# Kernel tuning notes

Measured on AMD Instinct MI355X. Metric: run time of the kernel, lower is better.

## Reference

```python
import jax, jax.numpy as jnp
import numpy as np

N_NODES = 50000
N_EDGES = 800000
IN_DIM = 128
HID = 64
NUM_GRAPHS = 64


def _gcn_conv(x, W, b, src, dst, num_nodes):
    """PyG GCNConv: out = D^-1/2 (A+I) D^-1/2 (x W) + b, messages scattered to dst."""
    h = x @ W  # [N, out]
    ones = jnp.ones((src.shape[0],), dtype=x.dtype)
    # degree at target nodes, self-loop adds 1
    deg = jax.ops.segment_sum(ones, dst, num_segments=num_nodes) + 1.0
    dinv = jax.lax.rsqrt(deg)  # [N]
    norm = dinv[src] * dinv[dst]  # [E]
    msgs = h[src] * norm[:, None]  # [E, out] gather-scale
    agg = jax.ops.segment_sum(msgs, dst, num_segments=num_nodes)  # scatter-add
    # self-loop contribution: norm_ii = dinv[i]^2
    agg = agg + h * (dinv * dinv)[:, None]
    return agg + b


def setup_inputs() -> dict:
    key = jax.random.key(0)
    k = jax.random.split(key, 10)
    x = jax.random.normal(k[0], (N_NODES, IN_DIM), dtype=jnp.float32)
    edge_index = jax.random.randint(k[1], (2, N_EDGES), 0, N_NODES, dtype=jnp.int32)
    batch = jnp.sort(jax.random.randint(k[2], (N_NODES,), 0, NUM_GRAPHS, dtype=jnp.int32))
    # Glorot-ish params
    W1 = jax.random.normal(k[3], (IN_DIM, HID), dtype=jnp.float32) / np.sqrt(IN_DIM)
    b1 = jnp.zeros((HID,), dtype=jnp.float32)
    W2 = jax.random.normal(k[4], (HID, HID), dtype=jnp.float32) / np.sqrt(HID)
    b2 = jnp.zeros((HID,), dtype=jnp.float32)
    Wlin = jax.random.normal(k[5], (HID, 1), dtype=jnp.float32) / np.sqrt(HID)
    blin = jnp.zeros((1,), dtype=jnp.float32)
    return {"x": x, "edge_index": edge_index, "batch": batch,
            "W1": W1, "b1": b1, "W2": W2, "b2": b2, "Wlin": Wlin, "blin": blin}


def reference(x, edge_index, batch, W1, b1, W2, b2, Wlin, blin):
    src, dst = edge_index[0], edge_index[1]
    h = _gcn_conv(x, W1, b1, src, dst, N_NODES)
    h = jax.nn.relu(h)  # dropout is identity in eval mode
    h = _gcn_conv(h, W2, b2, src, dst, N_NODES)
    h = jax.nn.relu(h)
    # global mean pool per graph
    sums = jax.ops.segment_sum(h, batch, num_segments=NUM_GRAPHS)  # [G, HID]
    cnts = jax.ops.segment_sum(jnp.ones((N_NODES,), h.dtype), batch, num_segments=NUM_GRAPHS)
    pooled = sums / jnp.maximum(cnts, 1.0)[:, None]
    return pooled @ Wlin + blin  # [G, 1]
```

## Files before the change

kernel.cpp:

```cpp
#include <hip/hip_runtime.h>
#include <hip/hip_fp16.h>

#define N_NODES 50000
#define N_EDGES 800000
#define IN_DIM 128
#define HID 64
#define NUM_GRAPHS 64
#define POOL_BLOCKS 512
#define NB 196
#define NBLK 256

__device__ inline float4 load_h4(const __half* p) {
    const __half2* q = (const __half2*)p;
    float2 a = __half22float2(q[0]);
    float2 b = __half22float2(q[1]);
    return make_float4(a.x, a.y, b.x, b.y);
}
__device__ inline void store_h4(__half* p, float4 v) {
    __half2* q = (__half2*)p;
    q[0] = __floats2half2_rn(v.x, v.y);
    q[1] = __floats2half2_rn(v.z, v.w);
}

__global__ __launch_bounds__(256) void hist_kernel(const int* __restrict__ dst, int* __restrict__ hist_g) {
    __shared__ int h[NB];
    int tid = threadIdx.x;
    for (int i = tid; i < NB; i += 256) h[i] = 0;
    __syncthreads();
    const int NI = N_EDGES / 4;
    for (int i = blockIdx.x * 256 + tid; i < NI; i += NBLK * 256) {
        int4 d = ((const int4*)dst)[i];
        atomicAdd(&h[d.x >> 8], 1);
        atomicAdd(&h[d.y >> 8], 1);
        atomicAdd(&h[d.z >> 8], 1);
        atomicAdd(&h[d.w >> 8], 1);
    }
    __syncthreads();
    for (int i = tid; i < NB; i += 256) hist_g[i * NBLK + blockIdx.x] = h[i];
}

__global__ __launch_bounds__(1024) void scan2_kernel(const int* __restrict__ in, int* __restrict__ pos,
                                                     int* __restrict__ offs) {
    __shared__ int wsum[16];
    __shared__ int tot_s;
    int tid = threadIdx.x;
    int lane = tid & 63, wid = tid >> 6;
    int carry = 0;
    const int L = NB * NBLK;
    for (int base = 0; base < L; base += 4096) {
        int idx = base + tid * 4;
        int v0 = 0, v1 = 0, v2 = 0, v3 = 0;
        if (idx < L) { int4 v = *(const int4*)&in[idx]; v0 = v.x; v1 = v.y; v2 = v.z; v3 = v.w; }
        int s0 = v0, s1 = s0 + v1, s2 = s1 + v2, s3 = s2 + v3;
        int inc = s3;
        #pragma unroll
        for (int d = 1; d < 64; d <<= 1) { int t = __shfl_up(inc, d, 64); if (lane >= d) inc += t; }
        if (lane == 63) wsum[wid] = inc;
        __syncthreads();
        if (tid < 16) {
            int wv = wsum[tid], winc = wv;
            #pragma unroll
            for (int d = 1; d < 16; d <<= 1) { int t = __shfl_up(winc, d, 16); if (tid >= d) winc += t; }
            wsum[tid] = winc - wv;
            if (tid == 15) tot_s = winc;
        }
        __syncthreads();
        int excl = carry + wsum[wid] + inc - s3;
        if (idx < L) { int4 o; o.x = excl; o.y = excl + s0; o.z = excl + s1; o.w = excl + s2; *(int4*)&pos[idx] = o; }
        carry += tot_s;
    }
    if (tid == 0) offs[N_NODES] = N_EDGES;
}

__global__ __launch_bounds__(256) void bin_kernel(const int* __restrict__ src, const int* __restrict__ dst,
                                                  const int* __restrict__ pos, int* __restrict__ binned) {
    __shared__ int cur[NB];
    int tid = threadIdx.x;
    for (int i = tid; i < NB; i += 256) cur[i] = pos[i * NBLK + blockIdx.x];
    __syncthreads();
    const int NI = N_EDGES / 4;
    for (int i = blockIdx.x * 256 + tid; i < NI; i += NBLK * 256) {
        int4 s = ((const int4*)src)[i];
        int4 d = ((const int4*)dst)[i];
        int p0 = atomicAdd(&cur[d.x >> 8], 1); binned[p0] = (s.x & 0xFFFF) | ((d.x & 255) << 16);
        int p1 = atomicAdd(&cur[d.y >> 8], 1); binned[p1] = (s.y & 0xFFFF) | ((d.y & 255) << 16);
        int p2 = atomicAdd(&cur[d.z >> 8], 1); binned[p2] = (s.z & 0xFFFF) | ((d.z & 255) << 16);
        int p3 = atomicAdd(&cur[d.w >> 8], 1); binned[p3] = (s.w & 0xFFFF) | ((d.w & 255) << 16);
    }
}

__global__ __launch_bounds__(256) void build_kernel(const int* __restrict__ binned, const int* __restrict__ pos,
                                                    int* __restrict__ offs, float* __restrict__ dinv,
                                                    int* __restrict__ csr_src) {
    __shared__ int cnt[256];
    __shared__ int excl[256];
    __shared__ int rnk[256];
    __shared__ int wtot[4];
    int b = blockIdx.x, tid = threadIdx.x;
    int base = pos[b * NBLK];
    int end  = (b == NB - 1) ? N_EDGES : pos[(b + 1) * NBLK];
    cnt[tid] = 0; rnk[tid] = 0;
    __syncthreads();
    for (int j = base + tid; j < end; j += 256) atomicAdd(&cnt[(binned[j] >> 16) & 255], 1);
    __syncthreads();
    int v = cnt[tid];
    int lane = tid & 63, wid = tid >> 6;
    int inc = v;
    #pragma unroll
    for (int d = 1; d < 64; d <<= 1) { int t = __shfl_up(inc, d, 64); if (lane >= d) inc += t; }
    if (lane == 63) wtot[wid] = inc;
    __syncthreads();
    if (tid == 0) {
        int a = 0;
        for (int w = 0; w < 4; w++) { int t = wtot[w]; wtot[w] = a; a += t; }
    }
    __syncthreads();
    excl[tid] = wtot[wid] + inc - v;
    int node = b * 256 + tid;
    if (node < N_NODES) {
        offs[node] = base + excl[tid];
        dinv[node] = rsqrtf((float)v + 1.0f);
    }
    __syncthreads();
    for (int j = base + tid; j < end; j += 256) {
        int e = binned[j];
        int l = (e >> 16) & 255;
        int r = atomicAdd(&rnk[l], 1);
        csr_src[base + excl[l] + r] = e & 0xFFFF;
    }
}

template <int K, typename TIN>
__global__ __launch_bounds__(256) void gemm_kernel(const TIN* __restrict__ A, const float* __restrict__ W,
                                                   const float* __restrict__ dinv,
                                                   __half* __restrict__ out, int nRows) {
    constexpr int KP = K + 4;
    __shared__ float xs[32 * KP];
    __shared__ float ws[K * 68];
    int tid = threadIdx.x;
    int node0 = blockIdx.x * 32;
    for (int i = tid; i < K * 16; i += 256) {
        int k = i >> 4, c4 = (i & 15) * 4;
        *(float4*)&ws[k * 68 + c4] = *(const float4*)&W[k * 64 + c4];
    }
    constexpr int K4 = K / 4;
    for (int i = tid; i < 32 * K4; i += 256) {
        int n = i / K4, k4 = i % K4;
        int gn = node0 + n;
        float4 v;
        if (gn < nRows) {
            if constexpr (sizeof(TIN) == 4) v = *(const float4*)&A[(size_t)gn * K + k4 * 4];
            else                            v = load_h4((const __half*)&A[(size_t)gn * K + k4 * 4]);
        } else v = make_float4(0.f, 0.f, 0.f, 0.f);
        *(float4*)&xs[n * KP + k4 * 4] = v;
    }
    __syncthreads();
    int tx4 = (tid & 15) * 4, ty = tid >> 4;
    int n0 = ty * 2;
    float acc[2][4] = {};
    for (int k = 0; k < K; k += 4) {
        float4 xv0 = *(const float4*)&xs[(n0 + 0) * KP + k];
        float4 xv1 = *(const float4*)&xs[(n0 + 1) * KP + k];
        #define GSTEP(X0, X1, KK) { \
            float4 wr = *(const float4*)&ws[(KK) * 68 + tx4]; \
            acc[0][0] += (X0) * wr.x; acc[0][1] += (X0) * wr.y; acc[0][2] += (X0) * wr.z; acc[0][3] += (X0) * wr.w; \
            acc[1][0] += (X1) * wr.x; acc[1][1] += (X1) * wr.y; acc[1][2] += (X1) * wr.z; acc[1][3] += (X1) * wr.w; }
        GSTEP(xv0.x, xv1.x, k + 0)
        GSTEP(xv0.y, xv1.y, k + 1)
        GSTEP(xv0.z, xv1.z, k + 2)
        GSTEP(xv0.w, xv1.w, k + 3)
        #undef GSTEP
    }
    #pragma unroll
    for (int i = 0; i < 2; i++) {
        int gn = node0 + n0 + i;
        if (gn < nRows) {
            float sc = dinv[gn];
            store_h4(&out[(size_t)gn * 64 + tx4],
                     make_float4(acc[i][0] * sc, acc[i][1] * sc, acc[i][2] * sc, acc[i][3] * sc));
        }
    }
}

__global__ __launch_bounds__(256) void agg_kernel(const __half* __restrict__ hd, const int* __restrict__ offs,
                                                  const int* __restrict__ csr_src,
                                                  const float* __restrict__ dinv, const float* __restrict__ bias,
                                                  __half* __restrict__ out) {
    int lane = threadIdx.x & 63;
    int node = blockIdx.x * 4 + (threadIdx.x >> 6);
    if (node >= N_NODES) return;
    int q = lane >> 4;
    int cc = (lane & 15) * 4;
    float4 acc = make_float4(0.f, 0.f, 0.f, 0.f);
    int beg = offs[node], end = offs[node + 1];
    #pragma unroll 2
    for (int j = beg + q; j < end; j += 4) {
        int s = csr_src[j];
        float4 hv = load_h4(&hd[(size_t)s * 64 + cc]);
        acc.x += hv.x; acc.y += hv.y; acc.z += hv.z; acc.w += hv.w;
    }
    #pragma unroll
    for (int m = 16; m <= 32; m <<= 1) {
        acc.x += __shfl_xor(acc.x, m, 64);
        acc.y += __shfl_xor(acc.y, m, 64);
        acc.z += __shfl_xor(acc.z, m, 64);
        acc.w += __shfl_xor(acc.w, m, 64);
    }
    if (q == 0) {
        float di = dinv[node];
        float4 hn = load_h4(&hd[(size_t)node * 64 + cc]);
        const float4 bv = *(const float4*)&bias[cc];
        float4 r;
        r.x = fmaxf(fmaf(di, acc.x + hn.x, bv.x), 0.0f);
        r.y = fmaxf(fmaf(di, acc.y + hn.y, bv.y), 0.0f);
        r.z = fmaxf(fmaf(di, acc.z + hn.z, bv.z), 0.0f);
        r.w = fmaxf(fmaf(di, acc.w + hn.w, bv.w), 0.0f);
        store_h4(&out[(size_t)node * 64 + cc], r);
    }
}

__global__ __launch_bounds__(256) void pool_kernel(const __half* __restrict__ y, const int* __restrict__ batch,
                                                   const float* __restrict__ Wlin,
                                                   float* __restrict__ gpart) {
    __shared__ float lsum[NUM_GRAPHS];
    __shared__ float lcnt[NUM_GRAPHS];
    int tid = threadIdx.x;
    if (tid < NUM_GRAPHS) { lsum[tid] = 0.0f; lcnt[tid] = 0.0f; }
    __syncthreads();
    int lane = tid & 63, wid = tid >> 6;
    int q = lane >> 4;
    int l16 = lane & 15;
    int cc = l16 * 4;
    float4 wl = *(const float4*)&Wlin[cc];
    int stride = gridDim.x * 16;
    #pragma unroll 2
    for (int node = blockIdx.x * 16 + wid * 4 + q; node < N_NODES; node += stride) {
        float4 v = load_h4(&y[(size_t)node * 64 + cc]);
        float d = v.x * wl.x + v.y * wl.y + v.z * wl.z + v.w * wl.w;
        #pragma unroll
        for (int m = 1; m < 16; m <<= 1) d += __shfl_xor(d, m, 64);
        if (l16 == 0) {
            int g = batch[node];
            atomicAdd(&lsum[g], d);
            atomicAdd(&lcnt[g], 1.0f);
        }
    }
    __syncthreads();
    if (tid < NUM_GRAPHS) {
        gpart[(size_t)blockIdx.x * (2 * NUM_GRAPHS) + tid] = lsum[tid];
        gpart[(size_t)blockIdx.x * (2 * NUM_GRAPHS) + NUM_GRAPHS + tid] = lcnt[tid];
    }
}

__global__ __launch_bounds__(1024) void final_kernel(const float* __restrict__ gpart, const float* __restrict__ blin,
                                                     float* __restrict__ out) {
    __shared__ float rs[1024];
    __shared__ float rc[1024];
    int tid = threadIdx.x;
    int g = tid & 63;
    int c = tid >> 6;
    float s = 0.0f, cn = 0.0f;
    for (int b = c; b < POOL_BLOCKS; b += 16) {
        s  += gpart[(size_t)b * (2 * NUM_GRAPHS) + g];
        cn += gpart[(size_t)b * (2 * NUM_GRAPHS) + NUM_GRAPHS + g];
    }
    rs[tid] = s; rc[tid] = cn;
    __syncthreads();
    if (c == 0) {
        float ts = 0.0f, tc = 0.0f;
        #pragma unroll
        for (int k = 0; k < 16; k++) { ts += rs[k * 64 + g]; tc += rc[k * 64 + g]; }
        out[g] = ts / fmaxf(tc, 1.0f) + blin[0];
    }
}

extern "C" void kernel_launch(void* const* d_in, const int* in_sizes, int n_in,
                              void* d_out, int out_size, void* d_ws, size_t ws_size,
                              hipStream_t stream) {
    const float* x    = (const float*)d_in[0];
    const int*   ei   = (const int*)d_in[1];
    const int*   batch= (const int*)d_in[2];
    const float* W1   = (const float*)d_in[3];
    const float* b1   = (const float*)d_in[4];
    const float* W2   = (const float*)d_in[5];
    const float* b2   = (const float*)d_in[6];
    const float* Wlin = (const float*)d_in[7];
    const float* blin = (const float*)d_in[8];
    float* out = (float*)d_out;
    const int* srcA = ei;
    const int* dstA = ei + N_EDGES;

    char* p = (char*)d_ws;
    auto alloc = [&](size_t n) { char* r = p; p += (n + 255) & ~(size_t)255; return r; };
    int*    hist_g  = (int*)alloc((size_t)NB * NBLK * 4);
    int*    pos     = (int*)alloc((size_t)NB * NBLK * 4);
    int*    offs    = (int*)alloc((size_t)(N_NODES + 1) * 4);
    int*    binned  = (int*)alloc((size_t)N_EDGES * 4);
    int*    csr_src = (int*)alloc((size_t)N_EDGES * 4);
    float*  dinv    = (float*)alloc((size_t)N_NODES * 4);
    float*  gpart   = (float*)alloc((size_t)POOL_BLOCKS * 2 * NUM_GRAPHS * 4);
    __half* bufA    = (__half*)alloc((size_t)N_NODES * 64 * 2);
    __half* bufB    = (__half*)alloc((size_t)N_NODES * 64 * 2);

    hist_kernel<<<NBLK, 256, 0, stream>>>(dstA, hist_g);
    scan2_kernel<<<1, 1024, 0, stream>>>(hist_g, pos, offs);
    bin_kernel<<<NBLK, 256, 0, stream>>>(srcA, dstA, pos, binned);
    build_kernel<<<NB, 256, 0, stream>>>(binned, pos, offs, dinv, csr_src);

    gemm_kernel<IN_DIM, float><<<(N_NODES + 31) / 32, 256, 0, stream>>>(x, W1, dinv, bufA, N_NODES);
    agg_kernel<<<(N_NODES + 3) / 4, 256, 0, stream>>>(bufA, offs, csr_src, dinv, b1, bufB);
    gemm_kernel<HID, __half><<<(N_NODES + 31) / 32, 256, 0, stream>>>(bufB, W2, dinv, bufA, N_NODES);
    agg_kernel<<<(N_NODES + 3) / 4, 256, 0, stream>>>(bufA, offs, csr_src, dinv, b2, bufB);

    pool_kernel<<<POOL_BLOCKS, 256, 0, stream>>>(bufB, batch, Wlin, gpart);
    final_kernel<<<1, 1024, 0, stream>>>(gpart, blin, out);
}
```

Before: 229.9 us.

## Fuse second aggregation with mean pooling and enlarge GEMM register tiles

```diff
diff --git a/kernel.cpp b/kernel.cpp
--- a/kernel.cpp
+++ b/kernel.cpp
@@ -6,7 +6,7 @@
 #define IN_DIM 128
 #define HID 64
 #define NUM_GRAPHS 64
-#define POOL_BLOCKS 512
+#define AGGP_BLOCKS 2048
 #define NB 196
 #define NBLK 256
 
@@ -134,50 +134,57 @@
 __global__ __launch_bounds__(256) void gemm_kernel(const TIN* __restrict__ A, const float* __restrict__ W,
                                                    const float* __restrict__ dinv,
                                                    __half* __restrict__ out, int nRows) {
-    constexpr int KP = K + 4;
-    __shared__ float xs[32 * KP];
-    __shared__ float ws[K * 68];
-    int tid = threadIdx.x;
-    int node0 = blockIdx.x * 32;
-    for (int i = tid; i < K * 16; i += 256) {
-        int k = i >> 4, c4 = (i & 15) * 4;
-        *(float4*)&ws[k * 68 + c4] = *(const float4*)&W[k * 64 + c4];
-    }
-    constexpr int K4 = K / 4;
-    for (int i = tid; i < 32 * K4; i += 256) {
-        int n = i / K4, k4 = i % K4;
-        int gn = node0 + n;
-        float4 v;
-        if (gn < nRows) {
-            if constexpr (sizeof(TIN) == 4) v = *(const float4*)&A[(size_t)gn * K + k4 * 4];
-            else                            v = load_h4((const __half*)&A[(size_t)gn * K + k4 * 4]);
-        } else v = make_float4(0.f, 0.f, 0.f, 0.f);
-        *(float4*)&xs[n * KP + k4 * 4] = v;
-    }
-    __syncthreads();
-    int tx4 = (tid & 15) * 4, ty = tid >> 4;
-    int n0 = ty * 2;
-    float acc[2][4] = {};
-    for (int k = 0; k < K; k += 4) {
-        float4 xv0 = *(const float4*)&xs[(n0 + 0) * KP + k];
-        float4 xv1 = *(const float4*)&xs[(n0 + 1) * KP + k];
-        #define GSTEP(X0, X1, KK) { \
-            float4 wr = *(const float4*)&ws[(KK) * 68 + tx4]; \
-            acc[0][0] += (X0) * wr.x; acc[0][1] += (X0) * wr.y; acc[0][2] += (X0) * wr.z; acc[0][3] += (X0) * wr.w; \
-            acc[1][0] += (X1) * wr.x; acc[1][1] += (X1) * wr.y; acc[1][2] += (X1) * wr.z; acc[1][3] += (X1) * wr.w; }
-        GSTEP(xv0.x, xv1.x, k + 0)
-        GSTEP(xv0.y, xv1.y, k + 1)
-        GSTEP(xv0.z, xv1.z, k + 2)
-        GSTEP(xv0.w, xv1.w, k + 3)
-        #undef GSTEP
+    constexpr int KB = 64;
+    __shared__ float xs[KB * 132];
+    __shared__ float ws[KB * 68];
+    int tid = threadIdx.x;
+    int node0 = blockIdx.x * 128;
+    int tx = tid & 7, ty = tid >> 3;
+    int c0 = tx * 8, n0 = ty * 4;
+    float acc[4][8] = {};
+    for (int kb = 0; kb < K; kb += KB) {
+        for (int i = tid; i < KB * 16; i += 256) {
+            int k = i >> 4, c4 = (i & 15) * 4;
+            *(float4*)&ws[k * 68 + c4] = *(const float4*)&W[(size_t)(kb + k) * 64 + c4];
+        }
+        for (int i = tid; i < 128 * (KB / 4); i += 256) {
+            int n = i / (KB / 4), k4 = (i % (KB / 4)) * 4;
+            int gn = node0 + n;
+            float4 v;
+            if (gn < nRows) {
+                if constexpr (sizeof(TIN) == 4) v = *(const float4*)&A[(size_t)gn * K + kb + k4];
+                else                            v = load_h4((const __half*)&A[(size_t)gn * K + kb + k4]);
+            } else v = make_float4(0.f, 0.f, 0.f, 0.f);
+            xs[(k4 + 0) * 132 + n] = v.x;
+            xs[(k4 + 1) * 132 + n] = v.y;
+            xs[(k4 + 2) * 132 + n] = v.z;
+            xs[(k4 + 3) * 132 + n] = v.w;
+        }
+        __syncthreads();
+        for (int k = 0; k < KB; k++) {
+            float4 xv = *(const float4*)&xs[k * 132 + n0];
+            float4 w0 = *(const float4*)&ws[k * 68 + c0];
+            float4 w1 = *(const float4*)&ws[k * 68 + c0 + 4];
+            #define NODE_FMA(i, X) \
+                acc[i][0] += (X) * w0.x; acc[i][1] += (X) * w0.y; acc[i][2] += (X) * w0.z; acc[i][3] += (X) * w0.w; \
+                acc[i][4] += (X) * w1.x; acc[i][5] += (X) * w1.y; acc[i][6] += (X) * w1.z; acc[i][7] += (X) * w1.w;
+            NODE_FMA(0, xv.x)
+            NODE_FMA(1, xv.y)
+            NODE_FMA(2, xv.z)
+            NODE_FMA(3, xv.w)
+            #undef NODE_FMA
+        }
+        __syncthreads();
     }
     #pragma unroll
-    for (int i = 0; i < 2; i++) {
+    for (int i = 0; i < 4; i++) {
         int gn = node0 + n0 + i;
         if (gn < nRows) {
             float sc = dinv[gn];
-            store_h4(&out[(size_t)gn * 64 + tx4],
+            store_h4(&out[(size_t)gn * 64 + c0],
                      make_float4(acc[i][0] * sc, acc[i][1] * sc, acc[i][2] * sc, acc[i][3] * sc));
+            store_h4(&out[(size_t)gn * 64 + c0 + 4],
+                     make_float4(acc[i][4] * sc, acc[i][5] * sc, acc[i][6] * sc, acc[i][7] * sc));
         }
     }
 }
@@ -219,9 +226,11 @@
     }
 }
 
-__global__ __launch_bounds__(256) void pool_kernel(const __half* __restrict__ y, const int* __restrict__ batch,
-                                                   const float* __restrict__ Wlin,
-                                                   float* __restrict__ gpart) {
+__global__ __launch_bounds__(256) void aggpool_kernel(const __half* __restrict__ hd, const int* __restrict__ offs,
+                                                      const int* __restrict__ csr_src,
+                                                      const float* __restrict__ dinv, const float* __restrict__ bias,
+                                                      const int* __restrict__ batch, const float* __restrict__ Wlin,
+                                                      float* __restrict__ gpart) {
     __shared__ float lsum[NUM_GRAPHS];
     __shared__ float lcnt[NUM_GRAPHS];
     int tid = threadIdx.x;
@@ -229,20 +238,41 @@
     __syncthreads();
     int lane = tid & 63, wid = tid >> 6;
     int q = lane >> 4;
-    int l16 = lane & 15;
-    int cc = l16 * 4;
-    float4 wl = *(const float4*)&Wlin[cc];
-    int stride = gridDim.x * 16;
-    #pragma unroll 2
-    for (int node = blockIdx.x * 16 + wid * 4 + q; node < N_NODES; node += stride) {
-        float4 v = load_h4(&y[(size_t)node * 64 + cc]);
-        float d = v.x * wl.x + v.y * wl.y + v.z * wl.z + v.w * wl.w;
+    int cc = (lane & 15) * 4;
+    const float4 wl = *(const float4*)&Wlin[cc];
+    int stride = gridDim.x * 4;
+    for (int node = blockIdx.x * 4 + wid; node < N_NODES; node += stride) {
+        float4 acc = make_float4(0.f, 0.f, 0.f, 0.f);
+        int beg = offs[node], end = offs[node + 1];
+        #pragma unroll 2
+        for (int j = beg + q; j < end; j += 4) {
+            int s = csr_src[j];
+            float4 hv = load_h4(&hd[(size_t)s * 64 + cc]);
+            acc.x += hv.x; acc.y += hv.y; acc.z += hv.z; acc.w += hv.w;
+        }
         #pragma unroll
-        for (int m = 1; m < 16; m <<= 1) d += __shfl_xor(d, m, 64);
-        if (l16 == 0) {
-            int g = batch[node];
-            atomicAdd(&lsum[g], d);
-            atomicAdd(&lcnt[g], 1.0f);
+        for (int m = 16; m <= 32; m <<= 1) {
+            acc.x += __shfl_xor(acc.x, m, 64);
+            acc.y += __shfl_xor(acc.y, m, 64);
+            acc.z += __shfl_xor(acc.z, m, 64);
+            acc.w += __shfl_xor(acc.w, m, 64);
+        }
+        if (q == 0) {
+            float di = dinv[node];
+            float4 hn = load_h4(&hd[(size_t)node * 64 + cc]);
+            const float4 bv = *(const float4*)&bias[cc];
+            float rx = fmaxf(fmaf(di, acc.x + hn.x, bv.x), 0.0f);
+            float ry = fmaxf(fmaf(di, acc.y + hn.y, bv.y), 0.0f);
+            float rz = fmaxf(fmaf(di, acc.z + hn.z, bv.z), 0.0f);
+            float rw = fmaxf(fmaf(di, acc.w + hn.w, bv.w), 0.0f);
+            float d = rx * wl.x + ry * wl.y + rz * wl.z + rw * wl.w;
+            #pragma unroll
+            for (int m = 1; m < 16; m <<= 1) d += __shfl_xor(d, m, 64);
+            if ((lane & 15) == 0) {
+                int g = batch[node];
+                atomicAdd(&lsum[g], d);
+                atomicAdd(&lcnt[g], 1.0f);
+            }
         }
     }
     __syncthreads();
@@ -260,7 +290,7 @@
     int g = tid & 63;
     int c = tid >> 6;
     float s = 0.0f, cn = 0.0f;
-    for (int b = c; b < POOL_BLOCKS; b += 16) {
+    for (int b = c; b < AGGP_BLOCKS; b += 16) {
         s  += gpart[(size_t)b * (2 * NUM_GRAPHS) + g];
         cn += gpart[(size_t)b * (2 * NUM_GRAPHS) + NUM_GRAPHS + g];
     }
@@ -298,7 +328,7 @@
     int*    binned  = (int*)alloc((size_t)N_EDGES * 4);
     int*    csr_src = (int*)alloc((size_t)N_EDGES * 4);
     float*  dinv    = (float*)alloc((size_t)N_NODES * 4);
-    float*  gpart   = (float*)alloc((size_t)POOL_BLOCKS * 2 * NUM_GRAPHS * 4);
+    float*  gpart   = (float*)alloc((size_t)AGGP_BLOCKS * 2 * NUM_GRAPHS * 4);
     __half* bufA    = (__half*)alloc((size_t)N_NODES * 64 * 2);
     __half* bufB    = (__half*)alloc((size_t)N_NODES * 64 * 2);
 
@@ -307,11 +337,10 @@
     bin_kernel<<<NBLK, 256, 0, stream>>>(srcA, dstA, pos, binned);
     build_kernel<<<NB, 256, 0, stream>>>(binned, pos, offs, dinv, csr_src);
 
-    gemm_kernel<IN_DIM, float><<<(N_NODES + 31) / 32, 256, 0, stream>>>(x, W1, dinv, bufA, N_NODES);
+    gemm_kernel<IN_DIM, float><<<(N_NODES + 127) / 128, 256, 0, stream>>>(x, W1, dinv, bufA, N_NODES);
     agg_kernel<<<(N_NODES + 3) / 4, 256, 0, stream>>>(bufA, offs, csr_src, dinv, b1, bufB);
-    gemm_kernel<HID, __half><<<(N_NODES + 31) / 32, 256, 0, stream>>>(bufB, W2, dinv, bufA, N_NODES);
-    agg_kernel<<<(N_NODES + 3) / 4, 256, 0, stream>>>(bufA, offs, csr_src, dinv, b2, bufB);
-
-    pool_kernel<<<POOL_BLOCKS, 256, 0, stream>>>(bufB, batch, Wlin, gpart);
+    gemm_kernel<HID, __half><<<(N_NODES + 127) / 128, 256, 0, stream>>>(bufB, W2, dinv, bufA, N_NODES);
+    aggpool_kernel<<<AGGP_BLOCKS, 256, 0, stream>>>(bufA, offs, csr_src, dinv, b2, batch, Wlin, gpart);
+
     final_kernel<<<1, 1024, 0, stream>>>(gpart, blin, out);
 }
```

After: 235.0 us. 1.02x slower.
